# Performance work log

Measured on AMD Instinct MI355X. Metric: run time of the kernel, lower is better.

The kernel has to match this reference:

```python
import jax, jax.numpy as jnp
import numpy as np

B, T, D, E, V = 16, 256, 512, 512, 32000  # batch, seqlen, embed_dim, encoder_embed_dim, vocab


def setup_inputs() -> dict:
    key = jax.random.key(0)
    ks = jax.random.split(key, 13)
    s = 0.05
    return {
        "prev_output_tokens": jax.random.randint(ks[0], (B, T), 0, V),
        "encoder_out": jax.random.normal(ks[1], (B, E), jnp.float32),
        "embed": jax.random.normal(ks[2], (V, D), jnp.float32) * s,
        "W_ih0": jax.random.normal(ks[3], (4 * D, E + D), jnp.float32) * s,
        "W_hh0": jax.random.normal(ks[4], (4 * D, D), jnp.float32) * s,
        "b_ih0": jax.random.normal(ks[5], (4 * D,), jnp.float32) * s,
        "b_hh0": jax.random.normal(ks[6], (4 * D,), jnp.float32) * s,
        "W_ih1": jax.random.normal(ks[7], (4 * D, D), jnp.float32) * s,
        "W_hh1": jax.random.normal(ks[8], (4 * D, D), jnp.float32) * s,
        "b_ih1": jax.random.normal(ks[9], (4 * D,), jnp.float32) * s,
        "b_hh1": jax.random.normal(ks[10], (4 * D,), jnp.float32) * s,
        "W_out": jax.random.normal(ks[11], (V, D), jnp.float32) * s,
        "b_out": jax.random.normal(ks[12], (V,), jnp.float32) * s,
    }


def _lstm_cell(x, h, c, W_ih, W_hh, b_ih, b_hh):
    # torch.nn.LSTMCell gate order: i, f, g, o
    gates = x @ W_ih.T + b_ih + h @ W_hh.T + b_hh
    i, f, g, o = jnp.split(gates, 4, axis=-1)
    c_new = jax.nn.sigmoid(f) * c + jax.nn.sigmoid(i) * jnp.tanh(g)
    h_new = jax.nn.sigmoid(o) * jnp.tanh(c_new)
    return h_new, c_new


def reference(prev_output_tokens, encoder_out, embed, W_ih0, W_hh0, b_ih0, b_hh0,
              W_ih1, W_hh1, b_ih1, b_hh1, W_out, b_out):
    # padding_idx=0 -> row 0 of the embedding table is zero
    embed = embed.at[0].set(0.0)
    x = embed[prev_output_tokens]          # [B, T, D]  (dropout: eval mode -> identity)
    x = jnp.swapaxes(x, 0, 1)              # [T, B, D]
    bsz = x.shape[1]
    h0 = jnp.zeros((bsz, W_hh0.shape[1]), x.dtype)
    c0, h1, c1 = h0, h0, h0

    def step(carry, x_t):
        h0, c0, h1, c1 = carry
        inp = jnp.concatenate([x_t, encoder_out], axis=1)   # [B, D+E]
        h0, c0 = _lstm_cell(inp, h0, c0, W_ih0, W_hh0, b_ih0, b_hh0)
        h1, c1 = _lstm_cell(h0, h1, c1, W_ih1, W_hh1, b_ih1, b_hh1)
        return (h0, c0, h1, c1), h1

    _, outs = jax.lax.scan(step, (h0, c0, h1, c1), x)       # outs: [T, B, D]
    outs = jnp.swapaxes(outs, 0, 1)                          # [B, T, D]
    return outs @ W_out.T + b_out                            # [B, T, V]
```

## Files before the change

kernel.cpp:

```cpp
#include <hip/hip_runtime.h>
#include <hip/hip_bf16.h>
#include <math.h>

#define BB 16
#define TT 256
#define DD 512
#define EE 512
#define VV 32000
#define G4 2048
#define NWORK 128
#define NTILES (16 * 2 * 250)

typedef __attribute__((ext_vector_type(4))) float f32x4;
typedef __attribute__((ext_vector_type(8))) short bf16x8;
typedef __attribute__((ext_vector_type(4))) unsigned u32x4;

union lf_u { u32x4 q; bf16x8 v; };

#define SENTMASK32 0x40004000u
#define SENTMASK64 0x4000400040004000ULL

__device__ __forceinline__ unsigned short f2bf(float x) {
    unsigned u = __float_as_uint(x);
    unsigned r = (u + 0x7FFFu + ((u >> 16) & 1u)) >> 16;
    return (unsigned short)r;
}

__device__ __forceinline__ float sigmoidf_(float x) { return 1.0f / (1.0f + expf(-x)); }

__global__ __launch_bounds__(256) void k_prep(
        const int* __restrict__ tok, const float* __restrict__ embed,
        unsigned short* __restrict__ Xb,
        const float* __restrict__ Wih0, unsigned short* __restrict__ Wih0xb,
        const float* __restrict__ enc, const float* __restrict__ bih0,
        const float* __restrict__ bhh0, float* __restrict__ et) {
    __shared__ float es[EE];
    const int blk = blockIdx.x;
    const int tid = threadIdx.x;
    if (blk < BB * TT) {
        int tk = tok[blk];
        const float* src = embed + (size_t)tk * DD;
        int i = tid * 2;
        float vx = 0.f, vy = 0.f;
        if (tk != 0) { float2 v = *(const float2*)&src[i]; vx = v.x; vy = v.y; }
        ushort2 o; o.x = f2bf(vx); o.y = f2bf(vy);
        *(ushort2*)&Xb[(size_t)blk * DD + i] = o;
    } else if (blk < BB * TT + 1024) {
        int i = (blk - BB * TT) * 256 + tid;
        int j = i >> 7;
        int k4 = (i & 127) << 2;
        float4 v = *(const float4*)&Wih0[(size_t)j * (EE + DD) + k4];
        ushort4 o; o.x = f2bf(v.x); o.y = f2bf(v.y); o.z = f2bf(v.z); o.w = f2bf(v.w);
        *(ushort4*)&Wih0xb[(size_t)j * DD + k4] = o;
    } else {
        int bidx = blk - (BB * TT + 1024);
        int b = bidx >> 3, jc = bidx & 7;
        int lane = tid & 63, w = tid >> 6;
        if (tid < EE / 4) *(float4*)&es[tid * 4] = *(const float4*)&enc[b * EE + tid * 4];
        __syncthreads();
        float4 e0 = *(const float4*)&es[lane * 4];
        float4 e1 = *(const float4*)&es[256 + lane * 4];
        for (int o = 0; o < 64; ++o) {
            int j = jc * 256 + w * 64 + o;
            const float4* Wr = (const float4*)&Wih0[(size_t)j * (EE + DD) + DD];
            float4 w0 = Wr[lane], w1 = Wr[64 + lane];
            float s = w0.x*e0.x + w0.y*e0.y + w0.z*e0.z + w0.w*e0.w
                    + w1.x*e1.x + w1.y*e1.y + w1.z*e1.z + w1.w*e1.w;
            #pragma unroll
            for (int off = 32; off; off >>= 1) s += __shfl_xor(s, off);
            if (lane == 0) et[b * G4 + j] = s + bih0[j] + bhh0[j];
        }
    }
}

__global__ __launch_bounds__(256) void k_gemm0(
        const unsigned short* __restrict__ A, const unsigned short* __restrict__ Bm,
        float* __restrict__ C, const float* __restrict__ extra,
        int M, int N, int K) {
    __shared__ __align__(16) unsigned short Alds[128 * 32];
    __shared__ __align__(16) unsigned short Blds[128 * 32];
    int tid = threadIdx.x, lane = tid & 63, w = tid >> 6;
    int wr = w >> 1, wc = w & 1;
    int nwgx = gridDim.x;
    int nwg = nwgx * gridDim.y;
    int lin = blockIdx.y * nwgx + blockIdx.x;
    int cpx = nwg >> 3;
    lin = (lin & 7) * cpx + (lin >> 3);
    int m0 = (lin % nwgx) * 128, n0 = (lin / nwgx) * 128;
    f32x4 acc[4][4];
    #pragma unroll
    for (int i = 0; i < 4; i++)
        #pragma unroll
        for (int j = 0; j < 4; j++) acc[i][j] = (f32x4)0.f;

    const char* Abase = (const char*)A;
    const char* Bbase = (const char*)Bm;
    for (int ks = 0; ks < K; ks += 32) {
        #pragma unroll
        for (int c = 0; c < 2; ++c) {
            int f = (tid + c * 256) * 16;
            int row = f >> 6;
            int inb = f & 63;
            const char* gA = Abase + (((size_t)(m0 + row) * K + ks) * 2 + inb);
            __builtin_amdgcn_global_load_lds(
                (const __attribute__((address_space(1))) void*)gA,
                (__attribute__((address_space(3))) void*)((char*)Alds + f), 16, 0, 0);
            const char* gB = Bbase + (((size_t)(n0 + row) * K + ks) * 2 + inb);
            __builtin_amdgcn_global_load_lds(
                (const __attribute__((address_space(1))) void*)gB,
                (__attribute__((address_space(3))) void*)((char*)Blds + f), 16, 0, 0);
        }
        __syncthreads();
        bf16x8 af[4], bfr[4];
        int r = lane & 15, ko = (lane >> 4) * 8;
        #pragma unroll
        for (int mi = 0; mi < 4; ++mi)
            af[mi] = *(const bf16x8*)&Alds[(wr * 64 + mi * 16 + r) * 32 + ko];
        #pragma unroll
        for (int ni = 0; ni < 4; ++ni)
            bfr[ni] = *(const bf16x8*)&Blds[(wc * 64 + ni * 16 + r) * 32 + ko];
        #pragma unroll
        for (int mi = 0; mi < 4; ++mi)
            #pragma unroll
            for (int ni = 0; ni < 4; ++ni)
                acc[mi][ni] = __builtin_amdgcn_mfma_f32_16x16x32_bf16(af[mi], bfr[ni], acc[mi][ni], 0, 0, 0);
        __syncthreads();
    }
    int cr = (lane >> 4) * 4, cc = lane & 15;
    #pragma unroll
    for (int mi = 0; mi < 4; ++mi) {
        #pragma unroll
        for (int ni = 0; ni < 4; ++ni) {
            int col = n0 + wc * 64 + ni * 16 + cc;
            #pragma unroll
            for (int rr = 0; rr < 4; ++rr) {
                int rowg = m0 + wr * 64 + mi * 16 + cr + rr;
                C[(size_t)rowg * N + col] = acc[mi][ni][rr] + extra[(rowg >> 8) * G4 + col];
            }
        }
    }
}

__device__ __forceinline__ void load16sc(const void* base, lf_u* o) {
    asm volatile(
        "global_load_dwordx4 %0, %16, off sc0 sc1\n\t"
        "global_load_dwordx4 %1, %16, off offset:64 sc0 sc1\n\t"
        "global_load_dwordx4 %2, %16, off offset:128 sc0 sc1\n\t"
        "global_load_dwordx4 %3, %16, off offset:192 sc0 sc1\n\t"
        "global_load_dwordx4 %4, %16, off offset:256 sc0 sc1\n\t"
        "global_load_dwordx4 %5, %16, off offset:320 sc0 sc1\n\t"
        "global_load_dwordx4 %6, %16, off offset:384 sc0 sc1\n\t"
        "global_load_dwordx4 %7, %16, off offset:448 sc0 sc1\n\t"
        "global_load_dwordx4 %8, %16, off offset:512 sc0 sc1\n\t"
        "global_load_dwordx4 %9, %16, off offset:576 sc0 sc1\n\t"
        "global_load_dwordx4 %10, %16, off offset:640 sc0 sc1\n\t"
        "global_load_dwordx4 %11, %16, off offset:704 sc0 sc1\n\t"
        "global_load_dwordx4 %12, %16, off offset:768 sc0 sc1\n\t"
        "global_load_dwordx4 %13, %16, off offset:832 sc0 sc1\n\t"
        "global_load_dwordx4 %14, %16, off offset:896 sc0 sc1\n\t"
        "global_load_dwordx4 %15, %16, off offset:960 sc0 sc1\n\t"
        "s_waitcnt vmcnt(0)"
        : "=&v"(o[0].q), "=&v"(o[1].q), "=&v"(o[2].q), "=&v"(o[3].q),
          "=&v"(o[4].q), "=&v"(o[5].q), "=&v"(o[6].q), "=&v"(o[7].q),
          "=&v"(o[8].q), "=&v"(o[9].q), "=&v"(o[10].q), "=&v"(o[11].q),
          "=&v"(o[12].q), "=&v"(o[13].q), "=&v"(o[14].q), "=&v"(o[15].q)
        : "v"(base)
        : "memory");
}

__device__ __forceinline__ void poll16sc(const void* base, lf_u* o) {
    for (;;) {
        load16sc(base, o);
        unsigned bad = 0;
        #pragma unroll
        for (int kt = 0; kt < 16; ++kt)
            bad |= (o[kt].q.x | o[kt].q.y | o[kt].q.z | o[kt].q.w);
        if (!__any((bad & SENTMASK32) != 0)) return;
        __builtin_amdgcn_s_sleep(1);
    }
}

__device__ __forceinline__ void store8sc(void* addr, unsigned long long v) {
    asm volatile("global_store_dwordx2 %0, %1, off sc0 sc1"
                 :: "v"(addr), "v"(v) : "memory");
}

__global__ __launch_bounds__(256) void k_mega(
        const float* __restrict__ Gx,
        const float* __restrict__ Whh0,
        const float* __restrict__ Wih1, const float* __restrict__ Whh1,
        const float* __restrict__ bih1, const float* __restrict__ bhh1,
        unsigned short* h0hist, unsigned short* outsb,
        const unsigned short* zbuf,
        const float* __restrict__ Wout, unsigned short* Woutb,
        const float* __restrict__ bout, float* __restrict__ out,
        int* ep1, int* tick, int* wdone) {
    __shared__ __align__(16) unsigned char smem[4 * 32 * 512 * 2 + 512];
    __shared__ int idSh;
    const int bid = blockIdx.x;

    if (bid < 64) {
        unsigned short* wfrag = (unsigned short*)smem;
        unsigned short* houts = (unsigned short*)(smem + 4 * 32 * 512 * 2);
        const int l = threadIdx.x;
        const int role = bid >> 5;
        const int blk = bid & 31;
        const int d0 = blk * 16;
        const int r16 = l & 15;
        const int q = (l >> 4) & 3;
        const int ksub = q * 8;
        const int b0 = q * 4;
        const int srow = (l >> 2) & 15;
        const int sseg = l & 3;

        const int nkt = role ? 32 : 16;
        if (l < 64) {
            for (int tile = 0; tile < 4; ++tile) {
                int j = tile * 512 + d0 + r16;
                for (int kt = 0; kt < nkt; ++kt) {
                    const float* src;
                    if (role == 0)    src = Whh0 + (size_t)j * DD + kt * 32 + ksub;
                    else if (kt < 16) src = Wih1 + (size_t)j * DD + kt * 32 + ksub;
                    else              src = Whh1 + (size_t)j * DD + (kt - 16) * 32 + ksub;
                    float4 x = *(const float4*)src;
                    float4 y = *(const float4*)(src + 4);
                    bf16x8 w;
                    w[0] = f2bf(x.x); w[1] = f2bf(x.y); w[2] = f2bf(x.z); w[3] = f2bf(x.w);
                    w[4] = f2bf(y.x); w[5] = f2bf(y.y); w[6] = f2bf(y.z); w[7] = f2bf(y.w);
                    *(bf16x8*)&wfrag[((tile * 32 + kt) * 64 + l) * 8] = w;
                }
            }
        }
        __syncthreads();

        if (l >= 64) {
            if (role == 1 && l < 128) {
                const int lw = l - 64;
                const int ob = lw >> 2;
                const int oseg = lw & 3;
                const char* base = (const char*)(outsb + ((size_t)ob * TT) * DD + d0 + oseg * 4);
                for (int t = 0; t < TT; ++t) {
                    const void* addr = base + (size_t)t * DD * 2;
                    for (;;) {
                        unsigned long long v;
                        asm volatile("global_load_dwordx2 %0, %1, off sc0 sc1\n\ts_waitcnt vmcnt(0)"
                                     : "=v"(v) : "v"(addr) : "memory");
                        if (!__any((v & SENTMASK64) != 0)) break;
                        __builtin_amdgcn_s_sleep(2);
                    }
                    if (lw == 0) {
                        int tv = t + 1;
                        asm volatile("global_store_dword %0, %1, off sc0 sc1"
                                     :: "v"(ep1 + blk * 16), "v"(tv) : "memory");
                    }
                }
            }
            return;
        }

        float cst[4] = {0.f, 0.f, 0.f, 0.f};
        lf_u xf[16];

        if (role == 0) {
            for (int t = 0; t < TT; ++t) {
                float gx[4][4];
                #pragma unroll
                for (int ni = 0; ni < 4; ++ni)
                    #pragma unroll
                    for (int rr = 0; rr < 4; ++rr)
                        gx[ni][rr] = Gx[((size_t)(b0 + rr) * TT + t) * G4 + ni * 512 + d0 + r16];

                const char* xb = (const char*)(h0hist + (size_t)t * (BB * DD) + r16 * DD) + q * 16;
                poll16sc(xb, xf);

                f32x4 acc[4];
                #pragma unroll
                for (int ni = 0; ni < 4; ++ni) acc[ni] = (f32x4)0.f;
                #pragma unroll
                for (int kt = 0; kt < 16; ++kt) {
                    #pragma unroll
                    for (int ni = 0; ni < 4; ++ni) {
                        bf16x8 wf = *(const bf16x8*)&wfrag[((ni * 32 + kt) * 64 + l) * 8];
                        acc[ni] = __builtin_amdgcn_mfma_f32_16x16x32_bf16(xf[kt].v, wf, acc[ni], 0, 0, 0);
                    }
                }
                #pragma unroll
                for (int rr = 0; rr < 4; ++rr) {
                    float gi = acc[0][rr] + gx[0][rr], gf = acc[1][rr] + gx[1][rr];
                    float gg = acc[2][rr] + gx[2][rr], go = acc[3][rr] + gx[3][rr];
                    float cn = sigmoidf_(gf) * cst[rr] + sigmoidf_(gi) * tanhf(gg);
                    float hn = sigmoidf_(go) * tanhf(cn);
                    cst[rr] = cn;
                    houts[(b0 + rr) * 16 + r16] = f2bf(hn);
                }
                asm volatile("" ::: "memory");
                {
                    const unsigned short* hp = &houts[srow * 16 + sseg * 4];
                    unsigned long long w8 =  (unsigned long long)hp[0]
                                          | ((unsigned long long)hp[1] << 16)
                                          | ((unsigned long long)hp[2] << 32)
                                          | ((unsigned long long)hp[3] << 48);
                    store8sc(h0hist + (size_t)(t + 1) * (BB * DD) + srow * DD + d0 + sseg * 4, w8);
                }
            }
        } else {
            lf_u hf[16];
            float bin[4];
            #pragma unroll
            for (int ni = 0; ni < 4; ++ni)
                bin[ni] = bih1[ni * 512 + d0 + r16] + bhh1[ni * 512 + d0 + r16];
            for (int t = 0; t < TT; ++t) {
                const char* xb = (const char*)(h0hist + (size_t)(t + 1) * (BB * DD) + r16 * DD) + q * 16;
                poll16sc(xb, xf);

                f32x4 acc[4];
                #pragma unroll
                for (int ni = 0; ni < 4; ++ni)
                    acc[ni] = (f32x4){bin[ni], bin[ni], bin[ni], bin[ni]};
                #pragma unroll
                for (int kt = 0; kt < 16; ++kt) {
                    #pragma unroll
                    for (int ni = 0; ni < 4; ++ni) {
                        bf16x8 wf = *(const bf16x8*)&wfrag[((ni * 32 + kt) * 64 + l) * 8];
                        acc[ni] = __builtin_amdgcn_mfma_f32_16x16x32_bf16(xf[kt].v, wf, acc[ni], 0, 0, 0);
                    }
                }
                const char* hb = (t == 0)
                    ? (const char*)(zbuf + r16 * DD) + q * 16
                    : (const char*)(outsb + ((size_t)r16 * TT + (t - 1)) * DD) + q * 16;
                poll16sc(hb, hf);
                #pragma unroll
                for (int kt = 0; kt < 16; ++kt) {
                    #pragma unroll
                    for (int ni = 0; ni < 4; ++ni) {
                        bf16x8 wf = *(const bf16x8*)&wfrag[((ni * 32 + 16 + kt) * 64 + l) * 8];
                        acc[ni] = __builtin_amdgcn_mfma_f32_16x16x32_bf16(hf[kt].v, wf, acc[ni], 0, 0, 0);
                    }
                }
                #pragma unroll
                for (int rr = 0; rr < 4; ++rr) {
                    float gi = acc[0][rr], gf = acc[1][rr], gg = acc[2][rr], go = acc[3][rr];
                    float cn = sigmoidf_(gf) * cst[rr] + sigmoidf_(gi) * tanhf(gg);
                    float hn = sigmoidf_(go) * tanhf(cn);
                    cst[rr] = cn;
                    houts[(b0 + rr) * 16 + r16] = f2bf(hn);
                }
                asm volatile("" ::: "memory");
                {
                    const unsigned short* hp = &houts[srow * 16 + sseg * 4];
                    unsigned long long w8 =  (unsigned long long)hp[0]
                                          | ((unsigned long long)hp[1] << 16)
                                          | ((unsigned long long)hp[2] << 32)
                                          | ((unsigned long long)hp[3] << 48);
                    store8sc(outsb + ((size_t)srow * TT + t) * DD + d0 + sseg * 4, w8);
                }
            }
        }
    } else if (bid < 64 + NWORK) {
        unsigned short* Alds = (unsigned short*)smem;
        unsigned short* Blds = (unsigned short*)(smem + 8192);
        const int tid = threadIdx.x, lane = tid & 63, w = tid >> 6;
        const int wr = w >> 1, wc = w & 1;
        const int wid = bid - 64;

        for (size_t i = (size_t)wid * 256 + tid; i < (size_t)VV * DD / 4;
             i += (size_t)NWORK * 256) {
            float4 v = ((const float4*)Wout)[i];
            unsigned long long pk =  (unsigned long long)f2bf(v.x)
                                  | ((unsigned long long)f2bf(v.y) << 16)
                                  | ((unsigned long long)f2bf(v.z) << 32)
                                  | ((unsigned long long)f2bf(v.w) << 48);
            store8sc(Woutb + i * 4, pk);
        }
        asm volatile("s_waitcnt vmcnt(0)" ::: "memory");
        if (tid == 0) {
            atomicAdd(wdone, 1);
            for (;;) {
                int v;
                asm volatile("global_load_dword %0, %1, off sc0 sc1\n\ts_waitcnt vmcnt(0)"
                             : "=v"(v) : "v"(wdone) : "memory");
                if (v >= NWORK) break;
                __builtin_amdgcn_s_sleep(8);
            }
        }
        __syncthreads();

        for (;;) {
            if (tid == 0) idSh = atomicAdd(tick, 1);
            __syncthreads();
            int id = idSh;
            if (id >= NTILES) break;

            int chunk = id / 500;
            int rem   = id % 500;
            int bg    = rem / 250;
            int nt    = rem % 250;
            int t0 = chunk * 16;
            int n0 = nt * 128;
            int target = t0 + 16;

            for (;;) {
                int v;
                asm volatile("global_load_dword %0, %1, off sc0 sc1\n\ts_waitcnt vmcnt(0)"
                             : "=v"(v) : "v"(ep1 + (lane & 31) * 16) : "memory");
                if (__all(v >= target)) break;
                __builtin_amdgcn_s_sleep(32);
            }

            f32x4 acc[4][4];
            #pragma unroll
            for (int i = 0; i < 4; i++)
                #pragma unroll
                for (int j = 0; j < 4; j++) acc[i][j] = (f32x4)0.f;

            for (int ks = 0; ks < DD; ks += 32) {
                #pragma unroll
                for (int c = 0; c < 2; ++c) {
                    int f = (tid + c * 256) * 16;
                    int row = f >> 6;
                    int inb = f & 63;
                    int bb = bg * 8 + (row >> 4);
                    int tt = t0 + (row & 15);
                    const char* gA = (const char*)outsb +
                        (((size_t)bb * TT + tt) * DD + ks) * 2 + inb;
                    __builtin_amdgcn_global_load_lds(
                        (const __attribute__((address_space(1))) void*)gA,
                        (__attribute__((address_space(3))) void*)((char*)Alds + f), 16, 0, 0);
                    const char* gB = (const char*)Woutb +
                        (((size_t)(n0 + row)) * DD + ks) * 2 + inb;
                    __builtin_amdgcn_global_load_lds(
                        (const __attribute__((address_space(1))) void*)gB,
                        (__attribute__((address_space(3))) void*)((char*)Blds + f), 16, 0, 0);
                }
                __syncthreads();
                bf16x8 af[4], bfr[4];
                int r = lane & 15, ko = (lane >> 4) * 8;
                #pragma unroll
                for (int mi = 0; mi < 4; ++mi)
                    af[mi] = *(const bf16x8*)&Alds[(wr * 64 + mi * 16 + r) * 32 + ko];
                #pragma unroll
                for (int ni = 0; ni < 4; ++ni)
                    bfr[ni] = *(const bf16x8*)&Blds[(wc * 64 + ni * 16 + r) * 32 + ko];
                #pragma unroll
                for (int mi = 0; mi < 4; ++mi)
                    #pragma unroll
                    for (int ni = 0; ni < 4; ++ni)
                        acc[mi][ni] = __builtin_amdgcn_mfma_f32_16x16x32_bf16(af[mi], bfr[ni], acc[mi][ni], 0, 0, 0);
                __syncthreads();
            }
            int cr = (lane >> 4) * 4, cc = lane & 15;
            #pragma unroll
            for (int mi = 0; mi < 4; ++mi) {
                #pragma unroll
                for (int ni = 0; ni < 4; ++ni) {
                    int col = n0 + wc * 64 + ni * 16 + cc;
                    #pragma unroll
                    for (int rr = 0; rr < 4; ++rr) {
                        int rloc = wr * 64 + mi * 16 + cr + rr;
                        int bb = bg * 8 + (rloc >> 4);
                        int tt = t0 + (rloc & 15);
                        out[((size_t)bb * TT + tt) * VV + col] = acc[mi][ni][rr] + bout[col];
                    }
                }
            }
        }
    }
}

extern "C" void kernel_launch(void* const* d_in, const int* in_sizes, int n_in,
                              void* d_out, int out_size, void* d_ws, size_t ws_size,
                              hipStream_t stream) {
    const int*   tok   = (const int*)  d_in[0];
    const float* enc   = (const float*)d_in[1];
    const float* embed = (const float*)d_in[2];
    const float* Wih0  = (const float*)d_in[3];
    const float* Whh0  = (const float*)d_in[4];
    const float* bih0  = (const float*)d_in[5];
    const float* bhh0  = (const float*)d_in[6];
    const float* Wih1  = (const float*)d_in[7];
    const float* Whh1  = (const float*)d_in[8];
    const float* bih1  = (const float*)d_in[9];
    const float* bhh1  = (const float*)d_in[10];
    const float* Wout  = (const float*)d_in[11];
    const float* bout  = (const float*)d_in[12];
    float* out = (float*)d_out;

    char* ws = (char*)d_ws;
    size_t off = 0;
    auto alloc = [&](size_t bytes) -> char* {
        char* p = ws + off; off += (bytes + 255) & ~(size_t)255; return p;
    };
    unsigned short* Xb     = (unsigned short*)alloc((size_t)BB * TT * DD * 2);
    unsigned short* Wih0xb = (unsigned short*)alloc((size_t)G4 * DD * 2);
    unsigned short* Woutb  = (unsigned short*)alloc((size_t)VV * DD * 2);
    float*          et     = (float*)alloc((size_t)BB * G4 * sizeof(float));
    float*          Gx     = (float*)alloc((size_t)BB * TT * G4 * sizeof(float));
    unsigned short* outsb  = (unsigned short*)alloc((size_t)BB * TT * DD * 2);
    unsigned short* h0hist = (unsigned short*)alloc((size_t)(TT + 1) * BB * DD * 2);
    unsigned short* zbuf   = (unsigned short*)alloc((size_t)BB * DD * 2);
    int*            ep1    = (int*)alloc(32 * 16 * sizeof(int));
    int*            tick   = (int*)alloc(64 * sizeof(int));
    int*            wdone  = (int*)alloc(64 * sizeof(int));

    hipMemsetAsync(h0hist, 0, (size_t)BB * DD * 2, stream);
    hipMemsetAsync(h0hist + (size_t)BB * DD, 0xFF, (size_t)TT * BB * DD * 2, stream);
    hipMemsetAsync(outsb, 0xFF, (size_t)BB * TT * DD * 2, stream);
    hipMemsetAsync(zbuf, 0, (size_t)BB * DD * 2, stream);
    hipMemsetAsync(ep1, 0, 32 * 16 * sizeof(int), stream);
    hipMemsetAsync(tick, 0, 64 * sizeof(int), stream);
    hipMemsetAsync(wdone, 0, 64 * sizeof(int), stream);

    k_prep<<<BB * TT + 1024 + 128, 256, 0, stream>>>(
        tok, embed, Xb, Wih0, Wih0xb, enc, bih0, bhh0, et);

    dim3 g1(BB * TT / 128, G4 / 128);
    k_gemm0<<<g1, 256, 0, stream>>>(Xb, Wih0xb, Gx, et, BB * TT, G4, DD);

    k_mega<<<256, 256, 0, stream>>>(Gx, Whh0, Wih1, Whh1, bih1, bhh1,
                                    h0hist, outsb, zbuf,
                                    Wout, Woutb, bout, out, ep1, tick, wdone);
}
```

Before: 1.528 ms.

## Widen layer-0 recurrence blocks to 32 hidden units, using 16 blocks instead of 32

Layer-0 LSTM recurrence now runs on 16 blocks, each owning 32 hidden units (8 MFMA tiles), instead of 32 blocks of 16 units. Each block stores its hidden-state slice with 16-byte stores. Fewer participating blocks means fewer cross-block polling agents and less coherence traffic per step on the serial critical path, at the cost of twice the MFMA work per block per step. Blocks 48-63 now do nothing.

Measured after the change: 1.907 ms. +24.8%, slower.

```diff
diff --git a/kernel.cpp b/kernel.cpp
--- a/kernel.cpp
+++ b/kernel.cpp
@@ -185,6 +185,14 @@
                  :: "v"(addr), "v"(v) : "memory");
 }
 
+__device__ __forceinline__ void store16sc(void* addr, unsigned long long lo, unsigned long long hi) {
+    u32x4 v;
+    v.x = (unsigned)lo; v.y = (unsigned)(lo >> 32);
+    v.z = (unsigned)hi; v.w = (unsigned)(hi >> 32);
+    asm volatile("global_store_dwordx4 %0, %1, off sc0 sc1"
+                 :: "v"(addr), "v"(v) : "memory");
+}
+
 __global__ __launch_bounds__(256) void k_mega(
         const float* __restrict__ Gx,
         const float* __restrict__ Whh0,
@@ -195,39 +203,50 @@
         const float* __restrict__ Wout, unsigned short* Woutb,
         const float* __restrict__ bout, float* __restrict__ out,
         int* ep1, int* tick, int* wdone) {
-    __shared__ __align__(16) unsigned char smem[4 * 32 * 512 * 2 + 512];
+    __shared__ __align__(16) unsigned char smem[4 * 32 * 512 * 2 + 1024];
     __shared__ int idSh;
     const int bid = blockIdx.x;
 
-    if (bid < 64) {
+    if (bid < 48) {
         unsigned short* wfrag = (unsigned short*)smem;
         unsigned short* houts = (unsigned short*)(smem + 4 * 32 * 512 * 2);
         const int l = threadIdx.x;
-        const int role = bid >> 5;
-        const int blk = bid & 31;
-        const int d0 = blk * 16;
+        const int role = (bid < 16) ? 0 : 1;
+        const int blk = role == 0 ? bid : bid - 16;
+        const int d0 = role == 0 ? blk * 32 : blk * 16;
         const int r16 = l & 15;
         const int q = (l >> 4) & 3;
         const int ksub = q * 8;
         const int b0 = q * 4;
-        const int srow = (l >> 2) & 15;
-        const int sseg = l & 3;
-
-        const int nkt = role ? 32 : 16;
+
         if (l < 64) {
-            for (int tile = 0; tile < 4; ++tile) {
-                int j = tile * 512 + d0 + r16;
-                for (int kt = 0; kt < nkt; ++kt) {
-                    const float* src;
-                    if (role == 0)    src = Whh0 + (size_t)j * DD + kt * 32 + ksub;
-                    else if (kt < 16) src = Wih1 + (size_t)j * DD + kt * 32 + ksub;
-                    else              src = Whh1 + (size_t)j * DD + (kt - 16) * 32 + ksub;
-                    float4 x = *(const float4*)src;
-                    float4 y = *(const float4*)(src + 4);
-                    bf16x8 w;
-                    w[0] = f2bf(x.x); w[1] = f2bf(x.y); w[2] = f2bf(x.z); w[3] = f2bf(x.w);
-                    w[4] = f2bf(y.x); w[5] = f2bf(y.y); w[6] = f2bf(y.z); w[7] = f2bf(y.w);
-                    *(bf16x8*)&wfrag[((tile * 32 + kt) * 64 + l) * 8] = w;
+            if (role == 0) {
+                for (int ti = 0; ti < 8; ++ti) {
+                    int j = (ti >> 1) * 512 + d0 + (ti & 1) * 16 + r16;
+                    for (int kt = 0; kt < 16; ++kt) {
+                        const float* src = Whh0 + (size_t)j * DD + kt * 32 + ksub;
+                        float4 x = *(const float4*)src;
+                        float4 y = *(const float4*)(src + 4);
+                        bf16x8 w;
+                        w[0] = f2bf(x.x); w[1] = f2bf(x.y); w[2] = f2bf(x.z); w[3] = f2bf(x.w);
+                        w[4] = f2bf(y.x); w[5] = f2bf(y.y); w[6] = f2bf(y.z); w[7] = f2bf(y.w);
+                        *(bf16x8*)&wfrag[((ti * 16 + kt) * 64 + l) * 8] = w;
+                    }
+                }
+            } else {
+                for (int tile = 0; tile < 4; ++tile) {
+                    int j = tile * 512 + d0 + r16;
+                    for (int kt = 0; kt < 32; ++kt) {
+                        const float* src = (kt < 16)
+                            ? Wih1 + (size_t)j * DD + kt * 32 + ksub
+                            : Whh1 + (size_t)j * DD + (kt - 16) * 32 + ksub;
+                        float4 x = *(const float4*)src;
+                        float4 y = *(const float4*)(src + 4);
+                        bf16x8 w;
+                        w[0] = f2bf(x.x); w[1] = f2bf(x.y); w[2] = f2bf(x.z); w[3] = f2bf(x.w);
+                        w[4] = f2bf(y.x); w[5] = f2bf(y.y); w[6] = f2bf(y.z); w[7] = f2bf(y.w);
+                        *(bf16x8*)&wfrag[((tile * 32 + kt) * 64 + l) * 8] = w;
+                    }
                 }
             }
         }
@@ -258,52 +277,66 @@
             return;
         }
 
-        float cst[4] = {0.f, 0.f, 0.f, 0.f};
         lf_u xf[16];
 
         if (role == 0) {
+            float cst[8] = {0.f, 0.f, 0.f, 0.f, 0.f, 0.f, 0.f, 0.f};
             for (int t = 0; t < TT; ++t) {
-                float gx[4][4];
-                #pragma unroll
-                for (int ni = 0; ni < 4; ++ni)
+                float gx[8][4];
+                #pragma unroll
+                for (int ti = 0; ti < 8; ++ti)
                     #pragma unroll
                     for (int rr = 0; rr < 4; ++rr)
-                        gx[ni][rr] = Gx[((size_t)(b0 + rr) * TT + t) * G4 + ni * 512 + d0 + r16];
+                        gx[ti][rr] = Gx[((size_t)(b0 + rr) * TT + t) * G4
+                                        + (ti >> 1) * 512 + d0 + (ti & 1) * 16 + r16];
 
                 const char* xb = (const char*)(h0hist + (size_t)t * (BB * DD) + r16 * DD) + q * 16;
                 poll16sc(xb, xf);
 
-                f32x4 acc[4];
-                #pragma unroll
-                for (int ni = 0; ni < 4; ++ni) acc[ni] = (f32x4)0.f;
+                f32x4 acc[8];
+                #pragma unroll
+                for (int ti = 0; ti < 8; ++ti) acc[ti] = (f32x4)0.f;
                 #pragma unroll
                 for (int kt = 0; kt < 16; ++kt) {
                     #pragma unroll
-                    for (int ni = 0; ni < 4; ++ni) {
-                        bf16x8 wf = *(const bf16x8*)&wfrag[((ni * 32 + kt) * 64 + l) * 8];
-                        acc[ni] = __builtin_amdgcn_mfma_f32_16x16x32_bf16(xf[kt].v, wf, acc[ni], 0, 0, 0);
+                    for (int ti = 0; ti < 8; ++ti) {
+                        bf16x8 wf = *(const bf16x8*)&wfrag[((ti * 16 + kt) * 64 + l) * 8];
+                        acc[ti] = __builtin_amdgcn_mfma_f32_16x16x32_bf16(xf[kt].v, wf, acc[ti], 0, 0, 0);
                     }
                 }
                 #pragma unroll
                 for (int rr = 0; rr < 4; ++rr) {
-                    float gi = acc[0][rr] + gx[0][rr], gf = acc[1][rr] + gx[1][rr];
-                    float gg = acc[2][rr] + gx[2][rr], go = acc[3][rr] + gx[3][rr];
-                    float cn = sigmoidf_(gf) * cst[rr] + sigmoidf_(gi) * tanhf(gg);
-                    float hn = sigmoidf_(go) * tanhf(cn);
-                    cst[rr] = cn;
-                    houts[(b0 + rr) * 16 + r16] = f2bf(hn);
+                    #pragma unroll
+                    for (int hf_ = 0; hf_ < 2; ++hf_) {
+                        float gi = acc[0 + hf_][rr] + gx[0 + hf_][rr];
+                        float gf = acc[2 + hf_][rr] + gx[2 + hf_][rr];
+                        float gg = acc[4 + hf_][rr] + gx[4 + hf_][rr];
+                        float go = acc[6 + hf_][rr] + gx[6 + hf_][rr];
+                        float cn = sigmoidf_(gf) * cst[rr * 2 + hf_] + sigmoidf_(gi) * tanhf(gg);
+                        float hn = sigmoidf_(go) * tanhf(cn);
+                        cst[rr * 2 + hf_] = cn;
+                        houts[(b0 + rr) * 32 + hf_ * 16 + r16] = f2bf(hn);
+                    }
                 }
                 asm volatile("" ::: "memory");
                 {
-                    const unsigned short* hp = &houts[srow * 16 + sseg * 4];
-                    unsigned long long w8 =  (unsigned long long)hp[0]
+                    const unsigned short* hp = &houts[(l >> 2) * 32 + (l & 3) * 8];
+                    unsigned long long lo =  (unsigned long long)hp[0]
                                           | ((unsigned long long)hp[1] << 16)
                                           | ((unsigned long long)hp[2] << 32)
                                           | ((unsigned long long)hp[3] << 48);
-                    store8sc(h0hist + (size_t)(t + 1) * (BB * DD) + srow * DD + d0 + sseg * 4, w8);
+                    unsigned long long hi =  (unsigned long long)hp[4]
+                                          | ((unsigned long long)hp[5] << 16)
+                                          | ((unsigned long long)hp[6] << 32)
+                                          | ((unsigned long long)hp[7] << 48);
+                    store16sc(h0hist + (size_t)(t + 1) * (BB * DD) + (l >> 2) * DD + d0 + (l & 3) * 8,
+                              lo, hi);
                 }
             }
         } else {
+            const int srow = (l >> 2) & 15;
+            const int sseg = l & 3;
+            float cst[4] = {0.f, 0.f, 0.f, 0.f};
             lf_u hf[16];
             float bin[4];
             #pragma unroll
@@ -356,7 +389,7 @@
                 }
             }
         }
-    } else if (bid < 64 + NWORK) {
+    } else if (bid >= 64 && bid < 64 + NWORK) {
         unsigned short* Alds = (unsigned short*)smem;
         unsigned short* Blds = (unsigned short*)(smem + 8192);
         const int tid = threadIdx.x, lane = tid & 63, w = tid >> 6;
```
